# Performance work log

Measured on AMD Instinct MI355X. Metric: run time of the kernel, lower is better.

## Reference

```python
import jax, jax.numpy as jnp
import numpy as np

B, T, D, H = 32, 2048, 1024, 16
HD = D // H
EPS = 1e-5


def _ln(x, g, b):
    mu = jnp.mean(x, axis=-1, keepdims=True)
    var = jnp.mean(jnp.square(x - mu), axis=-1, keepdims=True)
    return (x - mu) * jax.lax.rsqrt(var + EPS) * g + b


def setup_inputs() -> dict:
    key = jax.random.key(0)
    ks = jax.random.split(key, 6)
    return {
        "h_t": jax.random.normal(ks[0], (B, D), jnp.float32),
        "H_p": jax.random.normal(ks[1], (B, T, D), jnp.float32),
        "valid_len": jax.random.randint(ks[2], (B,), 1, T + 1, jnp.int32),
        "ln_q_g": jnp.ones((D,), jnp.float32),
        "ln_q_b": jnp.zeros((D,), jnp.float32),
        "ln_kv_g": jnp.ones((D,), jnp.float32),
        "ln_kv_b": jnp.zeros((D,), jnp.float32),
        "ln_out_g": jnp.ones((D,), jnp.float32),
        "ln_out_b": jnp.zeros((D,), jnp.float32),
        "log_tau": jnp.zeros((), jnp.float32),
        "in_proj_w": jax.random.normal(ks[3], (3 * D, D), jnp.float32) * 0.02,
        "in_proj_b": jnp.zeros((3 * D,), jnp.float32),
        "out_w": jax.random.normal(ks[4], (D, D), jnp.float32) * 0.02,
        "out_b": jnp.zeros((D,), jnp.float32),
    }


def reference(h_t, H_p, valid_len, ln_q_g, ln_q_b, ln_kv_g, ln_kv_b,
              ln_out_g, ln_out_b, log_tau, in_proj_w, in_proj_b, out_w, out_b):
    tau = jnp.clip(jnp.exp(log_tau), 0.25, 4.0)
    q = _ln(h_t, ln_q_g, ln_q_b) * tau            # (B, D)
    kv = _ln(H_p, ln_kv_g, ln_kv_b)               # (B, T, D)

    Wq, Wk, Wv = in_proj_w[:D], in_proj_w[D:2 * D], in_proj_w[2 * D:]
    bq, bk, bv = in_proj_b[:D], in_proj_b[D:2 * D], in_proj_b[2 * D:]

    qh = (q @ Wq.T + bq).reshape(B, H, HD)                         # (B, H, HD)
    kh = (jnp.einsum('btd,ed->bte', kv, Wk) + bk).reshape(B, T, H, HD)
    vh = (jnp.einsum('btd,ed->bte', kv, Wv) + bv).reshape(B, T, H, HD)

    scores = jnp.einsum('bhd,bthd->bht', qh, kh) / np.sqrt(HD)     # (B, H, T)
    pad = jnp.arange(T)[None, :] >= valid_len[:, None]             # (B, T) True = PAD
    scores = jnp.where(pad[:, None, :], -jnp.inf, scores)
    w = jax.nn.softmax(scores, axis=-1)

    ctx = jnp.einsum('bht,bthd->bhd', w, vh).reshape(B, D)
    ctx = ctx @ out_w.T + out_b
    return _ln(ctx + h_t, ln_out_g, ln_out_b)
```

## Files before the change

### kernel.cpp

```cpp
#include <hip/hip_runtime.h>
#include <math.h>

#define BB 32
#define TT 2048
#define DD 1024
#define NH 16
#define HDIM 64
#define EPS 1e-5f

__device__ __forceinline__ float wredSum(float v){
  v += __shfl_down(v, 32, 64);
  v += __shfl_down(v, 16, 64);
  v += __shfl_down(v, 8, 64);
  v += __shfl_down(v, 4, 64);
  v += __shfl_down(v, 2, 64);
  v += __shfl_down(v, 1, 64);
  return v;
}
__device__ float bredSum(float v, float* red){
  int lane = threadIdx.x & 63, w = threadIdx.x >> 6, nw = blockDim.x >> 6;
  v = wredSum(v);
  __syncthreads();
  if (lane == 0) red[w] = v;
  __syncthreads();
  if (w == 0){
    float x = (lane < nw) ? red[lane] : 0.f;
    x = wredSum(x);
    if (lane == 0) red[0] = x;
  }
  __syncthreads();
  return red[0];
}

__global__ __launch_bounds__(256) void k_qln(const float* __restrict__ h_t,
   const float* __restrict__ g, const float* __restrict__ bb,
   const float* __restrict__ log_tau, float* __restrict__ q)
{
  int b = blockIdx.x, tid = threadIdx.x;
  __shared__ float red[64];
  float4 x = ((const float4*)(h_t + (size_t)b*DD))[tid];
  float s = x.x + x.y + x.z + x.w;
  s = bredSum(s, red);
  float mu = s * (1.f/DD);
  float d0=x.x-mu, d1=x.y-mu, d2=x.z-mu, d3=x.w-mu;
  float s2 = d0*d0 + d1*d1 + d2*d2 + d3*d3;
  s2 = bredSum(s2, red);
  float rs = rsqrtf(s2*(1.f/DD) + EPS);
  float tau = fminf(fmaxf(expf(log_tau[0]), 0.25f), 4.0f);
  float4 gv = ((const float4*)g)[tid], bv = ((const float4*)bb)[tid];
  float4 o;
  o.x = (d0*rs*gv.x + bv.x)*tau;
  o.y = (d1*rs*gv.y + bv.y)*tau;
  o.z = (d2*rs*gv.z + bv.z)*tau;
  o.w = (d3*rs*gv.w + bv.w)*tau;
  ((float4*)(q + (size_t)b*DD))[tid] = o;
}

__global__ __launch_bounds__(256) void k_gemmsplit(const float* __restrict__ A,
    const float* __restrict__ W, float* __restrict__ p2)
{
  int ec = blockIdx.x, ds = blockIdx.y;
  int tid = threadIdx.x;
  __shared__ float Wl[64][132];
  __shared__ float Al[32][132];
  int d0 = ds*128, e0 = ec*64;
#pragma unroll
  for (int p=0;p<8;p++){
    int fi = p*256 + tid, r = fi >> 5, q4 = fi & 31;
    float4 v = *(const float4*)(W + (size_t)(e0+r)*DD + d0 + q4*4);
    *(float4*)&Wl[r][q4*4] = v;
  }
#pragma unroll
  for (int p=0;p<4;p++){
    int fi = p*256 + tid, r = fi >> 5, q4 = fi & 31;
    float4 v = *(const float4*)(A + (size_t)r*DD + d0 + q4*4);
    *(float4*)&Al[r][q4*4] = v;
  }
  __syncthreads();
  int eL = tid & 63, bg = tid >> 6;
  float acc[8];
#pragma unroll
  for (int i=0;i<8;i++) acc[i]=0.f;
  for (int d4=0; d4<32; d4++){
    float4 w = *(float4*)&Wl[eL][d4*4];
#pragma unroll
    for (int i=0;i<8;i++){
      float4 a = *(float4*)&Al[bg*8+i][d4*4];
      acc[i] = fmaf(w.x, a.x, acc[i]);
      acc[i] = fmaf(w.y, a.y, acc[i]);
      acc[i] = fmaf(w.z, a.z, acc[i]);
      acc[i] = fmaf(w.w, a.w, acc[i]);
    }
  }
#pragma unroll
  for (int i=0;i<8;i++)
    p2[((size_t)ds*BB + (bg*8+i))*DD + e0 + eL] = acc[i];
}

__global__ __launch_bounds__(256) void k_prep_s(const float* __restrict__ p2,
    const float* __restrict__ Wfull, const float* __restrict__ bfull,
    const float* __restrict__ g_kv, const float* __restrict__ b_kv,
    float* __restrict__ gs2, float* __restrict__ gsum, float* __restrict__ cst)
{
  int h = blockIdx.x, b = blockIdx.y;
  int tid = threadIdx.x;
  __shared__ float qhl[64];
  __shared__ float red[64];
  if (tid < 64){
    float s = bfull[h*HDIM + tid];
#pragma unroll
    for (int k=0;k<8;k++)
      s += p2[((size_t)k*BB + b)*DD + h*HDIM + tid];
    qhl[tid] = s;
  }
  __syncthreads();
  int d0 = tid*4;
  const float* Wk = Wfull + (size_t)DD*DD + (size_t)h*HDIM*DD + d0;
  float4 acc = make_float4(0.f,0.f,0.f,0.f);
#pragma unroll
  for (int j=0;j<64;j++){
    float qv = qhl[j];
    float4 w = *(const float4*)(Wk + (size_t)j*DD);
    acc.x = fmaf(qv, w.x, acc.x);
    acc.y = fmaf(qv, w.y, acc.y);
    acc.z = fmaf(qv, w.z, acc.z);
    acc.w = fmaf(qv, w.w, acc.w);
  }
  float4 gk = *(const float4*)(g_kv + d0);
  float4 bk = *(const float4*)(b_kv + d0);
  float4 gsv;
  gsv.x = acc.x*gk.x; gsv.y = acc.y*gk.y;
  gsv.z = acc.z*gk.z; gsv.w = acc.w*gk.w;
  int hq = h >> 2, hj = h & 3;
  float* gp = gs2 + (((size_t)b*4 + hq)*DD + d0)*4 + hj;
  gp[0] = gsv.x; gp[4] = gsv.y; gp[8] = gsv.z; gp[12] = gsv.w;
  float lgs = gsv.x + gsv.y + gsv.z + gsv.w;
  float lbs = acc.x*bk.x + acc.y*bk.y + acc.z*bk.z + acc.w*bk.w;
  float lc = 0.f;
  if (tid < 64) lc = qhl[tid] * bfull[DD + h*HDIM + tid];
  float tg = bredSum(lgs, red);
  float tb = bredSum(lbs + lc, red);
  if (tid == 0){ gsum[b*NH+h] = tg; cst[b*NH+h] = tb; }
}

#define SR 64
#define SDC 64
#define NCH (DD/SDC)
__global__ __launch_bounds__(256, 4) void k_scores(
    const float* __restrict__ X, const int* __restrict__ valid,
    const float* __restrict__ gs2, const float* __restrict__ gsum,
    const float* __restrict__ cst,
    float4* __restrict__ pacc, float* __restrict__ rs_arr,
    float* __restrict__ pm)
{
  int tc = blockIdx.x, b = blockIdx.y;
  int t0 = tc * SR;
  int vb = valid[b];
  if (t0 >= vb) return;
  int tid = threadIdx.x;
  int row = tid & 63, rx = row & 15;
  int hq = __builtin_amdgcn_readfirstlane(tid >> 6);
  __shared__ float4 xt[2][SR*16];
  __shared__ float4 gt[2][4*64];
  const float* xb = X + ((size_t)b*TT + t0)*DD;
  const float4* gq4 = (const float4*)gs2 + ((size_t)b*4 + hq)*DD;
  int r0 = tid >> 4, cg0 = tid & 15;
  float4 ld0, ld1, ld2, ld3, gld;
  float a0=0.f, a1=0.f, a2=0.f, a3=0.f, ssum=0.f, ssq=0.f;
#define LOADC(c) { const float* pb = xb + (c)*SDC; \
    ld0 = *(const float4*)(pb + (size_t)(r0+ 0)*DD + cg0*4); \
    ld1 = *(const float4*)(pb + (size_t)(r0+16)*DD + cg0*4); \
    ld2 = *(const float4*)(pb + (size_t)(r0+32)*DD + cg0*4); \
    ld3 = *(const float4*)(pb + (size_t)(r0+48)*DD + cg0*4); \
    gld = gq4[(c)*64 + row]; }
#define STOREC(c) { float4* tb2 = xt[(c)&1]; int u = cg0 ^ r0; \
    tb2[(r0+ 0)*16 + u] = ld0; \
    tb2[(r0+16)*16 + u] = ld1; \
    tb2[(r0+32)*16 + u] = ld2; \
    tb2[(r0+48)*16 + u] = ld3; \
    gt[(c)&1][hq*64 + row] = gld; }

  LOADC(0);
  STOREC(0);
  for (int c = 0; c < NCH; ++c){
    if (c+1 < NCH) LOADC(c+1);
    __syncthreads();
    {
      const float4* tb = xt[c&1] + row*16;
      const float4* gb = gt[c&1] + hq*64;
#pragma unroll 4
      for (int d4=0; d4<16; d4++){
        float4 xv = tb[d4 ^ rx];
        float4 g0 = gb[d4*4+0];
        float4 g1 = gb[d4*4+1];
        float4 g2 = gb[d4*4+2];
        float4 g3 = gb[d4*4+3];
        ssum += xv.x + xv.y + xv.z + xv.w;
        ssq = fmaf(xv.x,xv.x,ssq); ssq = fmaf(xv.y,xv.y,ssq);
        ssq = fmaf(xv.z,xv.z,ssq); ssq = fmaf(xv.w,xv.w,ssq);
        a0 = fmaf(xv.x,g0.x,a0); a1 = fmaf(xv.x,g0.y,a1);
        a2 = fmaf(xv.x,g0.z,a2); a3 = fmaf(xv.x,g0.w,a3);
        a0 = fmaf(xv.y,g1.x,a0); a1 = fmaf(xv.y,g1.y,a1);
        a2 = fmaf(xv.y,g1.z,a2); a3 = fmaf(xv.y,g1.w,a3);
        a0 = fmaf(xv.z,g2.x,a0); a1 = fmaf(xv.z,g2.y,a1);
        a2 = fmaf(xv.z,g2.z,a2); a3 = fmaf(xv.z,g2.w,a3);
        a0 = fmaf(xv.w,g3.x,a0); a1 = fmaf(xv.w,g3.y,a1);
        a2 = fmaf(xv.w,g3.z,a2); a3 = fmaf(xv.w,g3.w,a3);
      }
    }
    if (c+1 < NCH){
      __syncthreads();
      STOREC(c+1);
    }
  }
#undef LOADC
#undef STOREC
  float mu = ssum * (1.f/DD);
  float rs = rsqrtf(ssq*(1.f/DD) - mu*mu + EPS);
  int t = t0 + row;
  float4 gq = *(const float4*)(gsum + b*NH + hq*4);
  float4 cq = *(const float4*)(cst  + b*NH + hq*4);
  float4 sc;
  sc.x = (rs*(a0 - mu*gq.x) + cq.x)*0.125f;
  sc.y = (rs*(a1 - mu*gq.y) + cq.y)*0.125f;
  sc.z = (rs*(a2 - mu*gq.z) + cq.z)*0.125f;
  sc.w = (rs*(a3 - mu*gq.w) + cq.w)*0.125f;
  pacc[((size_t)b*4 + hq)*TT + t] = sc;
  if (hq == 0) rs_arr[(size_t)b*TT + t] = rs;

  bool act = (t < vb);
  float m0 = act ? sc.x : -3.0e38f;
  float m1 = act ? sc.y : -3.0e38f;
  float m2 = act ? sc.z : -3.0e38f;
  float m3 = act ? sc.w : -3.0e38f;
#pragma unroll
  for (int off=32; off>=1; off>>=1){
    m0 = fmaxf(m0, __shfl_xor(m0, off, 64));
    m1 = fmaxf(m1, __shfl_xor(m1, off, 64));
    m2 = fmaxf(m2, __shfl_xor(m2, off, 64));
    m3 = fmaxf(m3, __shfl_xor(m3, off, 64));
  }
  float rm = rs*mu;
  float e0 = act ? expf(sc.x - m0) : 0.f;
  float e1 = act ? expf(sc.y - m1) : 0.f;
  float e2 = act ? expf(sc.z - m2) : 0.f;
  float e3 = act ? expf(sc.w - m3) : 0.f;
  float S0=e0, S1=e1, S2=e2, S3=e3;
  float B0=e0*rm, B1=e1*rm, B2=e2*rm, B3=e3*rm;
#pragma unroll
  for (int off=32; off>=1; off>>=1){
    S0 += __shfl_xor(S0, off, 64);
    S1 += __shfl_xor(S1, off, 64);
    S2 += __shfl_xor(S2, off, 64);
    S3 += __shfl_xor(S3, off, 64);
    B0 += __shfl_xor(B0, off, 64);
    B1 += __shfl_xor(B1, off, 64);
    B2 += __shfl_xor(B2, off, 64);
    B3 += __shfl_xor(B3, off, 64);
  }
  if (row == 0){
    float* pb = pm + ((size_t)(b*(TT/SR) + tc)*3)*16 + hq*4;
    pb[0]=m0;  pb[1]=m1;  pb[2]=m2;  pb[3]=m3;
    pb[16]=S0; pb[17]=S1; pb[18]=S2; pb[19]=S3;
    pb[32]=B0; pb[33]=B1; pb[34]=B2; pb[35]=B3;
  }
}

#define BODY4(XC, Q0, Q1, Q2, Q3) { \
  float aa[16]={(Q0).x,(Q0).y,(Q0).z,(Q0).w,(Q1).x,(Q1).y,(Q1).z,(Q1).w, \
                (Q2).x,(Q2).y,(Q2).z,(Q2).w,(Q3).x,(Q3).y,(Q3).z,(Q3).w}; \
  _Pragma("unroll") \
  for (int h=0;h<16;h++){ ax[h]=fmaf(aa[h],(XC).x,ax[h]); ay[h]=fmaf(aa[h],(XC).y,ay[h]); } }

__global__ __launch_bounds__(512, 4) void k_accum(
    const float* __restrict__ X, const float4* __restrict__ pacc,
    const float* __restrict__ rs_arr, const float* __restrict__ pm,
    const int* __restrict__ valid, float* __restrict__ part, int ct)
{
  int c = blockIdx.x, b = blockIdx.y;
  int tid = threadIdx.x;
  int t0 = c*ct;
  int vb = valid[b];
  if (t0 >= vb) return;
  int tend = min(vb, t0 + ct);
  float ax[16], ay[16];
#pragma unroll
  for (int h=0;h<16;h++){ ax[h]=0.f; ay[h]=0.f; }
  __shared__ float4 at[2][256];
  __shared__ float mrg[3][32][16];
  __shared__ float mf[16], ivf[16];
  {
    int nch = (vb + SR - 1)/SR;
    int cc = tid >> 4, hh = tid & 15;
    float M=-3.0e38f, S=0.f, Bv=0.f;
    if (cc < nch){
      const float* pb = pm + ((size_t)(b*(TT/SR) + cc))*48;
      M = pb[hh]; S = pb[16+hh]; Bv = pb[32+hh];
    }
    mrg[0][cc][hh]=M; mrg[1][cc][hh]=S; mrg[2][cc][hh]=Bv;
    __syncthreads();
#pragma unroll
    for (int str=16; str>=1; str>>=1){
      if (cc < str){
        float ma=mrg[0][cc][hh], mbv=mrg[0][cc+str][hh];
        float Mn=fmaxf(ma,mbv);
        float f1=expf(ma-Mn), f2=expf(mbv-Mn);
        mrg[1][cc][hh]=mrg[1][cc][hh]*f1+mrg[1][cc+str][hh]*f2;
        mrg[2][cc][hh]=mrg[2][cc][hh]*f1+mrg[2][cc+str][hh]*f2;
        mrg[0][cc][hh]=Mn;
      }
      __syncthreads();
    }
    if (tid < 16){ mf[tid]=mrg[0][0][tid]; ivf[tid]=1.f/mrg[1][0][tid]; }
    __syncthreads();
  }
  const float2* xb = (const float2*)(X + (size_t)b*TT*DD);
  int tl6 = tid & 63, hqa = tid >> 6;
  float4 m4 = make_float4(0.f,0.f,0.f,0.f), iv4 = m4, scv = m4;
  float rsv = 0.f;
  if (tid < 256){
    m4  = make_float4(mf[hqa*4+0], mf[hqa*4+1], mf[hqa*4+2], mf[hqa*4+3]);
    iv4 = make_float4(ivf[hqa*4+0], ivf[hqa*4+1], ivf[hqa*4+2], ivf[hqa*4+3]);
    scv = pacc[((size_t)b*4 + hqa)*TT + t0 + tl6];
    rsv = rs_arr[(size_t)b*TT + t0 + tl6];
    float4 al;
    al.x = expf(scv.x - m4.x) * rsv * iv4.x;
    al.y = expf(scv.y - m4.y) * rsv * iv4.y;
    al.z = expf(scv.z - m4.z) * rsv * iv4.z;
    al.w = expf(scv.w - m4.w) * rsv * iv4.w;
    at[0][tl6*4 + hqa] = al;
  }
  int nsub = (tend - t0 + 63) >> 6;
  for (int s=0; s<nsub; s++){
    if (s+1 < nsub && tid < 256){
      int tn = t0 + (s+1)*64 + tl6;
      scv = pacc[((size_t)b*4 + hqa)*TT + tn];
      rsv = rs_arr[(size_t)b*TT + tn];
    }
    __syncthreads();
    int ts = t0 + s*64;
    int te = min(tend - ts, 64);
    const float4* av = at[s&1];
    if (te == 64){
      size_t rb = (size_t)ts*(DD/2) + tid;
      float2 x0 = xb[rb], x1 = xb[rb+512], x2 = xb[rb+1024], x3 = xb[rb+1536];
      for (int tl=0; tl<64; tl+=4){
        float2 c0=x0, c1=x1, c2=x2, c3=x3;
        if (tl < 60){
          size_t nb = rb + (size_t)(tl+4)*512;
          x0 = xb[nb]; x1 = xb[nb+512]; x2 = xb[nb+1024]; x3 = xb[nb+1536];
        }
        float4 p00=av[(tl+0)*4+0], p01=av[(tl+0)*4+1], p02=av[(tl+0)*4+2], p03=av[(tl+0)*4+3];
        BODY4(c0, p00, p01, p02, p03);
        float4 p10=av[(tl+1)*4+0], p11=av[(tl+1)*4+1], p12=av[(tl+1)*4+2], p13=av[(tl+1)*4+3];
        BODY4(c1, p10, p11, p12, p13);
        float4 p20=av[(tl+2)*4+0], p21=av[(tl+2)*4+1], p22=av[(tl+2)*4+2], p23=av[(tl+2)*4+3];
        BODY4(c2, p20, p21, p22, p23);
        float4 p30=av[(tl+3)*4+0], p31=av[(tl+3)*4+1], p32=av[(tl+3)*4+2], p33=av[(tl+3)*4+3];
        BODY4(c3, p30, p31, p32, p33);
      }
    } else {
      for (int tl=0; tl<te; tl++){
        float2 xc = xb[(size_t)(ts+tl)*(DD/2) + tid];
        float4 p0=av[tl*4+0], p1=av[tl*4+1], p2=av[tl*4+2], p3=av[tl*4+3];
        BODY4(xc, p0, p1, p2, p3);
      }
    }
    if (s+1 < nsub){
      __syncthreads();
      if (tid < 256){
        float4 al;
        al.x = expf(scv.x - m4.x) * rsv * iv4.x;
        al.y = expf(scv.y - m4.y) * rsv * iv4.y;
        al.z = expf(scv.z - m4.z) * rsv * iv4.z;
        al.w = expf(scv.w - m4.w) * rsv * iv4.w;
        at[(s+1)&1][tl6*4 + hqa] = al;
      }
    }
  }
  float* pp = part + (((size_t)c*BB + b)*NH)*DD;
#pragma unroll
  for (int h=0;h<16;h++)
    *(float2*)(pp + (size_t)h*DD + tid*2) = make_float2(ax[h], ay[h]);
}

__global__ __launch_bounds__(256) void k_uctx(const float* __restrict__ part,
   const int* __restrict__ valid, const float* __restrict__ pm,
   const float* __restrict__ g_kv, const float* __restrict__ b_kv,
   const float* __restrict__ Wfull, const float* __restrict__ bfull,
   float* __restrict__ ctx, int ct, int nc)
{
  int h = blockIdx.x, b = blockIdx.y;
  int tid = threadIdx.x;
  __shared__ float ul[DD];
  __shared__ float Wl[64][65];
  __shared__ float red2[4][64];
  __shared__ float bsh;
  int vb = valid[b];
  if (tid < 64){
    int nch = (vb + SR - 1)/SR;
    float M=-3.0e38f, S=0.f, Bv=0.f;
    if (tid < nch){
      const float* pb = pm + ((size_t)(b*(TT/SR) + tid))*48;
      M = pb[h]; S = pb[16+h]; Bv = pb[32+h];
    }
#pragma unroll
    for (int off=32; off>=1; off>>=1){
      float om = __shfl_down(M, off, 64);
      float oS = __shfl_down(S, off, 64);
      float oB = __shfl_down(Bv, off, 64);
      float Mn = fmaxf(M, om);
      float f1 = expf(M - Mn), f2 = expf(om - Mn);
      S  = S*f1 + oS*f2;
      Bv = Bv*f1 + oB*f2;
      M = Mn;
    }
    if (tid == 0) bsh = Bv * (1.f/S);
  }
  int nv = (vb + ct - 1) / ct;
  if (nv > nc) nv = nc;
  int d = tid*4;
  float4 s = make_float4(0.f,0.f,0.f,0.f);
  for (int c=0;c<nv;c++){
    float4 v = *(const float4*)(part + (((size_t)c*BB + b)*NH + h)*DD + d);
    s.x+=v.x; s.y+=v.y; s.z+=v.z; s.w+=v.w;
  }
  __syncthreads();
  {
    float be = bsh;
    float4 g = *(const float4*)(g_kv + d);
    float4 bv = *(const float4*)(b_kv + d);
    float4 r;
    r.x = fmaf(g.x, s.x-be, bv.x);
    r.y = fmaf(g.y, s.y-be, bv.y);
    r.z = fmaf(g.z, s.z-be, bv.z);
    r.w = fmaf(g.w, s.w-be, bv.w);
    ((float4*)ul)[tid] = r;
  }
  __syncthreads();
  int j = tid & 63, quart = tid >> 6;
  float acc = 0.f;
  const float* Wv = Wfull + (size_t)2*DD*DD;
  for (int dc=0; dc<DD; dc+=64){
#pragma unroll
    for (int p=0;p<4;p++){
      int fi = p*256 + tid, r = fi >> 4, q4 = fi & 15;
      float4 v = *(const float4*)(Wv + (size_t)(h*HDIM + r)*DD + dc + q4*4);
      Wl[r][q4*4+0]=v.x; Wl[r][q4*4+1]=v.y; Wl[r][q4*4+2]=v.z; Wl[r][q4*4+3]=v.w;
    }
    __syncthreads();
#pragma unroll
    for (int i=0;i<16;i++)
      acc = fmaf(Wl[j][quart*16+i], ul[dc + quart*16 + i], acc);
    __syncthreads();
  }
  red2[quart][j] = acc;
  __syncthreads();
  if (quart == 0){
    float v = red2[0][j] + red2[1][j] + red2[2][j] + red2[3][j];
    ctx[(size_t)b*DD + h*HDIM + j] = v + bfull[2*DD + h*HDIM + j];
  }
}

__global__ __launch_bounds__(256) void k_outln(const float* __restrict__ p2,
   const float* __restrict__ obias, const float* __restrict__ h_t,
   const float* __restrict__ g, const float* __restrict__ bb,
   float* __restrict__ out)
{
  int b = blockIdx.x, tid = threadIdx.x;
  __shared__ float red[64];
  int e = tid*4;
  float4 a = *(const float4*)(obias + e);
#pragma unroll
  for (int k=0;k<8;k++){
    float4 v = *(const float4*)(p2 + ((size_t)k*BB + b)*DD + e);
    a.x+=v.x; a.y+=v.y; a.z+=v.z; a.w+=v.w;
  }
  float4 r = ((const float4*)(h_t + (size_t)b*DD))[tid];
  a.x+=r.x; a.y+=r.y; a.z+=r.z; a.w+=r.w;
  float s = a.x + a.y + a.z + a.w;
  s = bredSum(s, red);
  float mu = s * (1.f/DD);
  float d0=a.x-mu, d1=a.y-mu, d2=a.z-mu, d3=a.w-mu;
  float s2 = d0*d0 + d1*d1 + d2*d2 + d3*d3;
  s2 = bredSum(s2, red);
  float rs = rsqrtf(s2*(1.f/DD) + EPS);
  float4 gv = ((const float4*)g)[tid], bv = ((const float4*)bb)[tid];
  float4 ov;
  ov.x = fmaf(d0*rs, gv.x, bv.x);
  ov.y = fmaf(d1*rs, gv.y, bv.y);
  ov.z = fmaf(d2*rs, gv.z, bv.z);
  ov.w = fmaf(d3*rs, gv.w, bv.w);
  ((float4*)(out + (size_t)b*DD))[tid] = ov;
}

extern "C" void kernel_launch(void* const* d_in, const int* in_sizes, int n_in,
                              void* d_out, int out_size, void* d_ws, size_t ws_size,
                              hipStream_t stream) {
  const float* h_t     = (const float*)d_in[0];
  const float* H_p     = (const float*)d_in[1];
  const int*   valid   = (const int*)  d_in[2];
  const float* ln_q_g  = (const float*)d_in[3];
  const float* ln_q_b  = (const float*)d_in[4];
  const float* ln_kv_g = (const float*)d_in[5];
  const float* ln_kv_b = (const float*)d_in[6];
  const float* ln_out_g= (const float*)d_in[7];
  const float* ln_out_b= (const float*)d_in[8];
  const float* log_tau = (const float*)d_in[9];
  const float* in_w    = (const float*)d_in[10];
  const float* in_b    = (const float*)d_in[11];
  const float* out_w   = (const float*)d_in[12];
  const float* out_b   = (const float*)d_in[13];
  float* out = (float*)d_out;

  float* ws     = (float*)d_ws;
  float* q      = ws;
  float* gs2    = q      + BB*DD;
  float* gsum   = gs2    + (size_t)BB*DD*NH;
  float* cst    = gsum   + BB*NH;
  float* ctx    = cst    + BB*NH;
  float* rs_arr = ctx    + BB*DD;
  float* pm     = rs_arr + (size_t)BB*TT;
  float* paccf  = pm     + (size_t)BB*(TT/SR)*48;
  float* part   = paccf  + (size_t)BB*4*TT*4;
  float4* pacc  = (float4*)paccf;

  size_t base_floats = (size_t)(part - ws);
  int nc = 16;
  if ((base_floats + (size_t)nc*BB*NH*DD) * sizeof(float) > ws_size) nc = 8;
  int ct = TT / nc;

  k_qln<<<BB, 256, 0, stream>>>(h_t, ln_q_g, ln_q_b, log_tau, q);
  k_gemmsplit<<<dim3(16,8), 256, 0, stream>>>(q, in_w, part);
  k_prep_s<<<dim3(NH,BB), 256, 0, stream>>>(part, in_w, in_b, ln_kv_g, ln_kv_b, gs2, gsum, cst);
  k_scores<<<dim3(TT/SR,BB), 256, 0, stream>>>(H_p, valid, gs2, gsum, cst, pacc, rs_arr, pm);
  k_accum<<<dim3(nc,BB), 512, 0, stream>>>(H_p, pacc, rs_arr, pm, valid, part, ct);
  k_uctx<<<dim3(NH,BB), 256, 0, stream>>>(part, valid, pm, ln_kv_g, ln_kv_b, in_w, in_b, ctx, ct, nc);
  k_gemmsplit<<<dim3(16,8), 256, 0, stream>>>(ctx, out_w, part);
  k_outln<<<BB, 256, 0, stream>>>(part, out_b, h_t, ln_out_g, ln_out_b, out);
}
```

Baseline: 147.2 us.

## Fuse weighted value accumulation into scores kernel with flash-style chunk rescaling

Removes the separate k_accum pass that re-read H_p. The scores kernel now computes each 64-row chunk's unnormalised exp weights times the LN scale into LDS, then accumulates weighted rows of X (still cached from the score pass) into per-chunk partials. k_uctx rescales and sums those per-chunk partials using the global max and sum, and its Wv tile width doubles to 128. This avoids a second full read of the 256MB H_p, at the cost of far more partial buffers (64 chunks × 16 heads × 1024 per batch) to write and reduce, plus a larger register footprint in k_scores.

```diff
diff --git a/kernel.cpp b/kernel.cpp
--- a/kernel.cpp
+++ b/kernel.cpp
@@ -150,8 +150,7 @@
     const float* __restrict__ X, const int* __restrict__ valid,
     const float* __restrict__ gs2, const float* __restrict__ gsum,
     const float* __restrict__ cst,
-    float4* __restrict__ pacc, float* __restrict__ rs_arr,
-    float* __restrict__ pm)
+    float* __restrict__ pm, float* __restrict__ part)
 {
   int tc = blockIdx.x, b = blockIdx.y;
   int t0 = tc * SR;
@@ -225,8 +224,6 @@
   sc.y = (rs*(a1 - mu*gq.y) + cq.y)*0.125f;
   sc.z = (rs*(a2 - mu*gq.z) + cq.z)*0.125f;
   sc.w = (rs*(a3 - mu*gq.w) + cq.w)*0.125f;
-  pacc[((size_t)b*4 + hq)*TT + t] = sc;
-  if (hq == 0) rs_arr[(size_t)b*TT + t] = rs;
 
   bool act = (t < vb);
   float m0 = act ? sc.x : -3.0e38f;
@@ -264,146 +261,61 @@
     pb[16]=S0; pb[17]=S1; pb[18]=S2; pb[19]=S3;
     pb[32]=B0; pb[33]=B1; pb[34]=B2; pb[35]=B3;
   }
-}
-
-#define BODY4(XC, Q0, Q1, Q2, Q3) { \
-  float aa[16]={(Q0).x,(Q0).y,(Q0).z,(Q0).w,(Q1).x,(Q1).y,(Q1).z,(Q1).w, \
-                (Q2).x,(Q2).y,(Q2).z,(Q2).w,(Q3).x,(Q3).y,(Q3).z,(Q3).w}; \
-  _Pragma("unroll") \
-  for (int h=0;h<16;h++){ ax[h]=fmaf(aa[h],(XC).x,ax[h]); ay[h]=fmaf(aa[h],(XC).y,ay[h]); } }
-
-__global__ __launch_bounds__(512, 4) void k_accum(
-    const float* __restrict__ X, const float4* __restrict__ pacc,
-    const float* __restrict__ rs_arr, const float* __restrict__ pm,
-    const int* __restrict__ valid, float* __restrict__ part, int ct)
-{
-  int c = blockIdx.x, b = blockIdx.y;
-  int tid = threadIdx.x;
-  int t0 = c*ct;
-  int vb = valid[b];
-  if (t0 >= vb) return;
-  int tend = min(vb, t0 + ct);
-  float ax[16], ay[16];
-#pragma unroll
-  for (int h=0;h<16;h++){ ax[h]=0.f; ay[h]=0.f; }
-  __shared__ float4 at[2][256];
-  __shared__ float mrg[3][32][16];
-  __shared__ float mf[16], ivf[16];
-  {
-    int nch = (vb + SR - 1)/SR;
-    int cc = tid >> 4, hh = tid & 15;
-    float M=-3.0e38f, S=0.f, Bv=0.f;
-    if (cc < nch){
-      const float* pb = pm + ((size_t)(b*(TT/SR) + cc))*48;
-      M = pb[hh]; S = pb[16+hh]; Bv = pb[32+hh];
-    }
-    mrg[0][cc][hh]=M; mrg[1][cc][hh]=S; mrg[2][cc][hh]=Bv;
-    __syncthreads();
-#pragma unroll
-    for (int str=16; str>=1; str>>=1){
-      if (cc < str){
-        float ma=mrg[0][cc][hh], mbv=mrg[0][cc+str][hh];
-        float Mn=fmaxf(ma,mbv);
-        float f1=expf(ma-Mn), f2=expf(mbv-Mn);
-        mrg[1][cc][hh]=mrg[1][cc][hh]*f1+mrg[1][cc+str][hh]*f2;
-        mrg[2][cc][hh]=mrg[2][cc][hh]*f1+mrg[2][cc+str][hh]*f2;
-        mrg[0][cc][hh]=Mn;
-      }
-      __syncthreads();
-    }
-    if (tid < 16){ mf[tid]=mrg[0][0][tid]; ivf[tid]=1.f/mrg[1][0][tid]; }
-    __syncthreads();
-  }
-  const float2* xb = (const float2*)(X + (size_t)b*TT*DD);
-  int tl6 = tid & 63, hqa = tid >> 6;
-  float4 m4 = make_float4(0.f,0.f,0.f,0.f), iv4 = m4, scv = m4;
-  float rsv = 0.f;
-  if (tid < 256){
-    m4  = make_float4(mf[hqa*4+0], mf[hqa*4+1], mf[hqa*4+2], mf[hqa*4+3]);
-    iv4 = make_float4(ivf[hqa*4+0], ivf[hqa*4+1], ivf[hqa*4+2], ivf[hqa*4+3]);
-    scv = pacc[((size_t)b*4 + hqa)*TT + t0 + tl6];
-    rsv = rs_arr[(size_t)b*TT + t0 + tl6];
-    float4 al;
-    al.x = expf(scv.x - m4.x) * rsv * iv4.x;
-    al.y = expf(scv.y - m4.y) * rsv * iv4.y;
-    al.z = expf(scv.z - m4.z) * rsv * iv4.z;
-    al.w = expf(scv.w - m4.w) * rsv * iv4.w;
-    at[0][tl6*4 + hqa] = al;
-  }
-  int nsub = (tend - t0 + 63) >> 6;
-  for (int s=0; s<nsub; s++){
-    if (s+1 < nsub && tid < 256){
-      int tn = t0 + (s+1)*64 + tl6;
-      scv = pacc[((size_t)b*4 + hqa)*TT + tn];
-      rsv = rs_arr[(size_t)b*TT + tn];
-    }
-    __syncthreads();
-    int ts = t0 + s*64;
-    int te = min(tend - ts, 64);
-    const float4* av = at[s&1];
-    if (te == 64){
-      size_t rb = (size_t)ts*(DD/2) + tid;
-      float2 x0 = xb[rb], x1 = xb[rb+512], x2 = xb[rb+1024], x3 = xb[rb+1536];
-      for (int tl=0; tl<64; tl+=4){
-        float2 c0=x0, c1=x1, c2=x2, c3=x3;
-        if (tl < 60){
-          size_t nb = rb + (size_t)(tl+4)*512;
-          x0 = xb[nb]; x1 = xb[nb+512]; x2 = xb[nb+1024]; x3 = xb[nb+1536];
-        }
-        float4 p00=av[(tl+0)*4+0], p01=av[(tl+0)*4+1], p02=av[(tl+0)*4+2], p03=av[(tl+0)*4+3];
-        BODY4(c0, p00, p01, p02, p03);
-        float4 p10=av[(tl+1)*4+0], p11=av[(tl+1)*4+1], p12=av[(tl+1)*4+2], p13=av[(tl+1)*4+3];
-        BODY4(c1, p10, p11, p12, p13);
-        float4 p20=av[(tl+2)*4+0], p21=av[(tl+2)*4+1], p22=av[(tl+2)*4+2], p23=av[(tl+2)*4+3];
-        BODY4(c2, p20, p21, p22, p23);
-        float4 p30=av[(tl+3)*4+0], p31=av[(tl+3)*4+1], p32=av[(tl+3)*4+2], p33=av[(tl+3)*4+3];
-        BODY4(c3, p30, p31, p32, p33);
-      }
-    } else {
-      for (int tl=0; tl<te; tl++){
-        float2 xc = xb[(size_t)(ts+tl)*(DD/2) + tid];
-        float4 p0=av[tl*4+0], p1=av[tl*4+1], p2=av[tl*4+2], p3=av[tl*4+3];
-        BODY4(xc, p0, p1, p2, p3);
-      }
-    }
-    if (s+1 < nsub){
-      __syncthreads();
-      if (tid < 256){
-        float4 al;
-        al.x = expf(scv.x - m4.x) * rsv * iv4.x;
-        al.y = expf(scv.y - m4.y) * rsv * iv4.y;
-        al.z = expf(scv.z - m4.z) * rsv * iv4.z;
-        al.w = expf(scv.w - m4.w) * rsv * iv4.w;
-        at[(s+1)&1][tl6*4 + hqa] = al;
-      }
-    }
-  }
-  float* pp = part + (((size_t)c*BB + b)*NH)*DD;
+
+  float* alds = (float*)gt;
+  alds[(hq*4+0)*64 + row] = e0 * rs;
+  alds[(hq*4+1)*64 + row] = e1 * rs;
+  alds[(hq*4+2)*64 + row] = e2 * rs;
+  alds[(hq*4+3)*64 + row] = e3 * rs;
+  __syncthreads();
+
+  float4 u[16];
+#pragma unroll
+  for (int h=0;h<16;h++) u[h] = make_float4(0.f,0.f,0.f,0.f);
+  const float4* xr4 = (const float4*)xb;
+  float4 xv = xr4[tid];
+  for (int tl=0; tl<64; tl++){
+    float4 cur = xv;
+    if (tl < 63) xv = xr4[(tl+1)*256 + tid];
+    float av[16];
+#pragma unroll
+    for (int h=0;h<16;h++) av[h] = alds[h*64 + tl];
+#pragma unroll
+    for (int h=0;h<16;h++){
+      u[h].x = fmaf(av[h], cur.x, u[h].x);
+      u[h].y = fmaf(av[h], cur.y, u[h].y);
+      u[h].z = fmaf(av[h], cur.z, u[h].z);
+      u[h].w = fmaf(av[h], cur.w, u[h].w);
+    }
+  }
+  float* pp = part + ((size_t)(tc*BB + b)*NH)*DD;
 #pragma unroll
   for (int h=0;h<16;h++)
-    *(float2*)(pp + (size_t)h*DD + tid*2) = make_float2(ax[h], ay[h]);
+    ((float4*)(pp + (size_t)h*DD))[tid] = u[h];
 }
 
 __global__ __launch_bounds__(256) void k_uctx(const float* __restrict__ part,
    const int* __restrict__ valid, const float* __restrict__ pm,
    const float* __restrict__ g_kv, const float* __restrict__ b_kv,
    const float* __restrict__ Wfull, const float* __restrict__ bfull,
-   float* __restrict__ ctx, int ct, int nc)
+   float* __restrict__ ctx)
 {
   int h = blockIdx.x, b = blockIdx.y;
   int tid = threadIdx.x;
   __shared__ float ul[DD];
-  __shared__ float Wl[64][65];
+  __shared__ float Wl[64][133];
   __shared__ float red2[4][64];
+  __shared__ float wc[TT/SR];
   __shared__ float bsh;
   int vb = valid[b];
+  int nch = (vb + SR - 1)/SR;
   if (tid < 64){
-    int nch = (vb + SR - 1)/SR;
-    float M=-3.0e38f, S=0.f, Bv=0.f;
+    float M0=-3.0e38f, S=0.f, Bv=0.f;
     if (tid < nch){
       const float* pb = pm + ((size_t)(b*(TT/SR) + tid))*48;
-      M = pb[h]; S = pb[16+h]; Bv = pb[32+h];
-    }
+      M0 = pb[h]; S = pb[16+h]; Bv = pb[32+h];
+    }
+    float M = M0;
 #pragma unroll
     for (int off=32; off>=1; off>>=1){
       float om = __shfl_down(M, off, 64);
@@ -415,17 +327,23 @@
       Bv = Bv*f1 + oB*f2;
       M = Mn;
     }
-    if (tid == 0) bsh = Bv * (1.f/S);
-  }
-  int nv = (vb + ct - 1) / ct;
-  if (nv > nc) nv = nc;
+    float Mt = __shfl(M, 0, 64);
+    float St = __shfl(S, 0, 64);
+    float Bt = __shfl(Bv, 0, 64);
+    if (tid < nch) wc[tid] = expf(M0 - Mt) / St;
+    if (tid == 0) bsh = Bt / St;
+  }
+  __syncthreads();
   int d = tid*4;
   float4 s = make_float4(0.f,0.f,0.f,0.f);
-  for (int c=0;c<nv;c++){
+  for (int c=0;c<nch;c++){
+    float w = wc[c];
     float4 v = *(const float4*)(part + (((size_t)c*BB + b)*NH + h)*DD + d);
-    s.x+=v.x; s.y+=v.y; s.z+=v.z; s.w+=v.w;
-  }
-  __syncthreads();
+    s.x = fmaf(w, v.x, s.x);
+    s.y = fmaf(w, v.y, s.y);
+    s.z = fmaf(w, v.z, s.z);
+    s.w = fmaf(w, v.w, s.w);
+  }
   {
     float be = bsh;
     float4 g = *(const float4*)(g_kv + d);
@@ -441,17 +359,17 @@
   int j = tid & 63, quart = tid >> 6;
   float acc = 0.f;
   const float* Wv = Wfull + (size_t)2*DD*DD;
-  for (int dc=0; dc<DD; dc+=64){
-#pragma unroll
-    for (int p=0;p<4;p++){
-      int fi = p*256 + tid, r = fi >> 4, q4 = fi & 15;
+  for (int dc=0; dc<DD; dc+=128){
+#pragma unroll
+    for (int p=0;p<8;p++){
+      int fi = p*256 + tid, r = fi >> 5, q4 = fi & 31;
       float4 v = *(const float4*)(Wv + (size_t)(h*HDIM + r)*DD + dc + q4*4);
       Wl[r][q4*4+0]=v.x; Wl[r][q4*4+1]=v.y; Wl[r][q4*4+2]=v.z; Wl[r][q4*4+3]=v.w;
     }
     __syncthreads();
 #pragma unroll
-    for (int i=0;i<16;i++)
-      acc = fmaf(Wl[j][quart*16+i], ul[dc + quart*16 + i], acc);
+    for (int i=0;i<32;i++)
+      acc = fmaf(Wl[j][quart*32+i], ul[dc + quart*32 + i], acc);
     __syncthreads();
   }
   red2[quart][j] = acc;
@@ -519,23 +437,14 @@
   float* gsum   = gs2    + (size_t)BB*DD*NH;
   float* cst    = gsum   + BB*NH;
   float* ctx    = cst    + BB*NH;
-  float* rs_arr = ctx    + BB*DD;
-  float* pm     = rs_arr + (size_t)BB*TT;
-  float* paccf  = pm     + (size_t)BB*(TT/SR)*48;
-  float* part   = paccf  + (size_t)BB*4*TT*4;
-  float4* pacc  = (float4*)paccf;
-
-  size_t base_floats = (size_t)(part - ws);
-  int nc = 16;
-  if ((base_floats + (size_t)nc*BB*NH*DD) * sizeof(float) > ws_size) nc = 8;
-  int ct = TT / nc;
+  float* pm     = ctx    + BB*DD;
+  float* part   = pm     + (size_t)BB*(TT/SR)*48;
 
   k_qln<<<BB, 256, 0, stream>>>(h_t, ln_q_g, ln_q_b, log_tau, q);
   k_gemmsplit<<<dim3(16,8), 256, 0, stream>>>(q, in_w, part);
   k_prep_s<<<dim3(NH,BB), 256, 0, stream>>>(part, in_w, in_b, ln_kv_g, ln_kv_b, gs2, gsum, cst);
-  k_scores<<<dim3(TT/SR,BB), 256, 0, stream>>>(H_p, valid, gs2, gsum, cst, pacc, rs_arr, pm);
-  k_accum<<<dim3(nc,BB), 512, 0, stream>>>(H_p, pacc, rs_arr, pm, valid, part, ct);
-  k_uctx<<<dim3(NH,BB), 256, 0, stream>>>(part, valid, pm, ln_kv_g, ln_kv_b, in_w, in_b, ctx, ct, nc);
+  k_scores<<<dim3(TT/SR,BB), 256, 0, stream>>>(H_p, valid, gs2, gsum, cst, pm, part);
+  k_uctx<<<dim3(NH,BB), 256, 0, stream>>>(part, valid, pm, ln_kv_g, ln_kv_b, in_w, in_b, ctx);
   k_gemmsplit<<<dim3(16,8), 256, 0, stream>>>(ctx, out_w, part);
   k_outln<<<BB, 256, 0, stream>>>(part, out_b, h_t, ln_out_g, ln_out_b, out);
 }
```

Measured after the change: 253.3 us. 1.72x slower.
